# Optimization experiments

Hardware: AMD Instinct MI355X
Metric: run time of the kernel (lower is better)

The kernel has to match this reference:

```python
import jax, jax.numpy as jnp
import numpy as np

B, T, C = 4, 4096, 512
H = 64           # head_size
GRAN = 128       # staircase granularity


def staircase_mask(t, g):
    # tril OR block-diagonal blocks of size g (the staircase fills the upper
    # triangle inside each gxg diagonal block)
    i = jnp.arange(t)
    return (i[:, None] >= i[None, :]) | ((i[:, None] // g) == (i[None, :] // g))


def setup_inputs() -> dict:
    key = jax.random.key(0)
    kx, kk, kq, kv = jax.random.split(key, 4)
    scale = 0.02
    return {
        "x": jax.random.normal(kx, (B, T, C), dtype=jnp.float32),
        "Wk": jax.random.normal(kk, (C, H), dtype=jnp.float32) * scale,
        "Wq": jax.random.normal(kq, (C, H), dtype=jnp.float32) * scale,
        "Wv": jax.random.normal(kv, (C, H), dtype=jnp.float32) * scale,
    }


def reference(x, Wk, Wq, Wv):
    # single head of self-attention with staircase mask (dropout off / eval mode)
    k = x @ Wk          # [B,T,H]
    q = x @ Wq          # [B,T,H]
    v = x @ Wv          # [B,T,H]
    wei = jnp.einsum("bth,bsh->bts", q, k) * (H ** -0.5)   # [B,T,T]
    mask = staircase_mask(T, GRAN)                           # [T,T] bool
    wei = jnp.where(mask, wei, -jnp.inf)
    wei = jax.nn.softmax(wei, axis=-1)
    out = jnp.einsum("bts,bsh->bth", wei, v)                 # [B,T,H]
    return out
```

## Files before the change

kernel.cpp:

```cpp
#include <hip/hip_runtime.h>

typedef unsigned short u16;
typedef unsigned int u32;
typedef unsigned long long u64;
typedef __attribute__((ext_vector_type(8))) short short8;
typedef __attribute__((ext_vector_type(4))) float f32x4;

#define T_ 4096
#define QSCALE 0.18033688f
#define CH 4
#define SBAT 576
#define PSTRIDE 36

#if __has_builtin(__builtin_amdgcn_exp2f)
#define EXP2F(x) __builtin_amdgcn_exp2f(x)
#else
#define EXP2F(x) exp2f(x)
#endif

__device__ __forceinline__ u16 f2bf(float f) {
    unsigned u = __float_as_uint(f);
    u += 0x7FFFu + ((u >> 16) & 1u);
    return (u16)(u >> 16);
}

__global__ __launch_bounds__(256) void wtrans_kernel(
    const float* __restrict__ Wq, const float* __restrict__ Wk,
    const float* __restrict__ Wv, u16* __restrict__ WTf)
{
    const int tid  = blockIdx.x * 256 + threadIdx.x;
    const int frag = tid >> 6;
    const int lane = tid & 63;
    const int ng   = frag >> 4;
    const int kc   = frag & 15;
    const int m    = ng >> 2;
    const float* W = (m == 0) ? Wq : (m == 1) ? Wk : Wv;
    const int h  = (ng & 3) * 16 + (lane & 15);
    const int c0 = kc * 32 + (lane >> 4) * 8;
    short8 v;
    #pragma unroll
    for (int j = 0; j < 8; ++j)
        v[j] = (short)f2bf(W[(c0 + j) * 64 + h]);
    *(short8*)(WTf + (size_t)frag * 512 + lane * 8) = v;
}

__global__ __launch_bounds__(256) void proj_kernel(
    const float* __restrict__ x, const u16* __restrict__ WTf,
    u16* __restrict__ Qf, u16* __restrict__ Kf, u16* __restrict__ Vf)
{
    __shared__ u16 xs[16 * 520];
    __shared__ u16 img[3072];
    const int t    = threadIdx.x;
    const int lane = t & 63;
    const int w    = t >> 6;
    const int l16  = lane & 15;
    const int quad = lane >> 4;
    const int rowbase = blockIdx.x * 16;
    const int bat  = rowbase >> 12;
    const int tloc = rowbase & 4095;

    #pragma unroll
    for (int it = 0; it < 8; ++it) {
        int f   = t + it * 256;
        int row = f >> 7;
        int c4  = (f & 127) * 4;
        f32x4 a = *(const f32x4*)(x + (size_t)(rowbase + row) * 512 + c4);
        unsigned lo = (unsigned)f2bf(a[0]) | ((unsigned)f2bf(a[1]) << 16);
        unsigned hi = (unsigned)f2bf(a[2]) | ((unsigned)f2bf(a[3]) << 16);
        *(uint2*)(xs + row * 520 + c4) = make_uint2(lo, hi);
    }
    __syncthreads();

    f32x4 acc[3];
    #pragma unroll
    for (int nt = 0; nt < 3; ++nt) acc[nt] = (f32x4){0.f, 0.f, 0.f, 0.f};

    const u16* ab = xs + l16 * 520 + quad * 8;
    const u16* wb = WTf + (size_t)(w * 3 * 16) * 512 + lane * 8;

    #pragma unroll 4
    for (int kc = 0; kc < 16; ++kc) {
        short8 af = *(const short8*)(ab + kc * 32);
        #pragma unroll
        for (int nt = 0; nt < 3; ++nt) {
            short8 bf = *(const short8*)(wb + (size_t)(nt * 16 + kc) * 512);
            acc[nt] = __builtin_amdgcn_mfma_f32_16x16x32_bf16(af, bf, acc[nt], 0, 0, 0);
        }
    }

    #pragma unroll
    for (int nt = 0; nt < 3; ++nt) {
        int ng = w * 3 + nt;
        if (ng < 8) {
            int ng4  = ng & 3;
            float sc = (ng < 4) ? QSCALE : 1.0f;
            u16* ib  = img + ((ng < 4) ? 0 : 1024) + (ng4 >> 1) * 512
                          + ((ng4 & 1) * 2 + (l16 >> 3)) * 128 + (l16 & 7);
            #pragma unroll
            for (int i = 0; i < 4; ++i)
                ib[(quad * 4 + i) * 8] = f2bf(acc[nt][i] * sc);
        } else {
            int nt2  = ng - 8;
            unsigned lo = (unsigned)f2bf(acc[nt][0]) | ((unsigned)f2bf(acc[nt][1]) << 16);
            unsigned hi = (unsigned)f2bf(acc[nt][2]) | ((unsigned)f2bf(acc[nt][3]) << 16);
            *(uint2*)(img + 2048 + nt2 * 256 + (quad >> 1) * 128 + l16 * 8
                          + (quad & 1) * 4) = make_uint2(lo, hi);
        }
    }
    __syncthreads();

    const int tb   = tloc >> 4;
    const int kt   = tloc >> 7;
    const int ks   = (tloc >> 5) & 3;
    const int half = (tloc >> 4) & 1;
    uint2 vq = *(uint2*)(img + t * 4);
    uint2 vk = *(uint2*)(img + 1024 + t * 4);
    uint2 vv = *(uint2*)(img + 2048 + t * 4);
    *(uint2*)(Qf + (size_t)(bat * 256 + tb) * 1024 + t * 4) = vq;
    *(uint2*)(Kf + (size_t)(bat * 256 + tb) * 1024 + t * 4) = vk;
    const int nt2c = t >> 6;
    *(uint2*)(Vf + (size_t)((bat * 32 + kt) * 4 + ks) * 2048
                 + nt2c * 512 + half * 256 + (t & 63) * 4) = vv;
}

__global__ __launch_bounds__(256, 4) void attn_kernel(
    const u16* __restrict__ Qf, const u16* __restrict__ Kf,
    const u16* __restrict__ Vf, u32* __restrict__ pnum,
    float* __restrict__ pden, float* __restrict__ out)
{
    __shared__ u16 Ps[4][2][2][16 * PSTRIDE];

    const int w    = threadIdx.x >> 6;
    const int lane = threadIdx.x & 63;
    const int l16  = lane & 15;
    const int qd   = lane >> 4;
    const int xcd  = blockIdx.x & 7;
    const int bat  = xcd >> 1;
    const int tw   = ((blockIdx.x >> 3) * 2 + (xcd & 1)) * 4 + w;

    int A = 31, pre = 0, cc = 1;
    for (;;) {
        cc = (A + CH) / CH;
        int cnt4 = 4 * cc;
        if (tw < pre + cnt4) break;
        pre += cnt4; --A;
    }
    const int r    = tw - pre;
    const int c    = r >> 2;
    const int b_   = r & 3;
    const int nkt  = A + 1;
    const int q32  = 4 * A + b_;
    const int kt0  = c * CH;
    const int kt1  = min(kt0 + CH, nkt);
    const int slot = bat * SBAT + pre + b_ + 4 * c;

    short8 aq[2][2];
    #pragma unroll
    for (int g = 0; g < 2; ++g)
        #pragma unroll
        for (int f = 0; f < 2; ++f)
            aq[g][f] = *(const short8*)(Qf
                + ((size_t)((bat * 256 + q32 * 2 + g) * 2 + f)) * 512 + lane * 8);

    short8 ones;
    #pragma unroll
    for (int j = 0; j < 8; ++j) ones[j] = (short)0x3F80;

    f32x4 acc[2][4];
    f32x4 accden[2];
    #pragma unroll
    for (int g = 0; g < 2; ++g) {
        accden[g] = (f32x4){0.f, 0.f, 0.f, 0.f};
        for (int n = 0; n < 4; ++n) acc[g][n] = (f32x4){0.f, 0.f, 0.f, 0.f};
    }

    u16* Psw = &Ps[w][0][0][0];
    int par = 0;

    short8 ap_prev[2];
    short8 av_prev[4];

    auto step = [&](int kt, int ks, bool first) __attribute__((always_inline)) {
        const u16* kfb = Kf + ((size_t)(bat * 256 + kt * 8) * 2) * 512 + lane * 8;
        const u16* vfb = Vf + ((size_t)((bat * 32 + kt) * 16)) * 512 + lane * 8;
        f32x4 st0g0, st0g1, st1g0, st1g1;
        {
            short8 k0 = *(const short8*)(kfb + (size_t)(2 * ks) * 1024);
            short8 k1 = *(const short8*)(kfb + (size_t)(2 * ks) * 1024 + 512);
            f32x4 s;
            s = (f32x4){0.f, 0.f, 0.f, 0.f};
            s = __builtin_amdgcn_mfma_f32_16x16x32_bf16(k0, aq[0][0], s, 0, 0, 0);
            s = __builtin_amdgcn_mfma_f32_16x16x32_bf16(k1, aq[0][1], s, 0, 0, 0);
            st0g0 = s;
            s = (f32x4){0.f, 0.f, 0.f, 0.f};
            s = __builtin_amdgcn_mfma_f32_16x16x32_bf16(k0, aq[1][0], s, 0, 0, 0);
            s = __builtin_amdgcn_mfma_f32_16x16x32_bf16(k1, aq[1][1], s, 0, 0, 0);
            st0g1 = s;
        }
        {
            short8 k0 = *(const short8*)(kfb + (size_t)(2 * ks + 1) * 1024);
            short8 k1 = *(const short8*)(kfb + (size_t)(2 * ks + 1) * 1024 + 512);
            f32x4 s;
            s = (f32x4){0.f, 0.f, 0.f, 0.f};
            s = __builtin_amdgcn_mfma_f32_16x16x32_bf16(k0, aq[0][0], s, 0, 0, 0);
            s = __builtin_amdgcn_mfma_f32_16x16x32_bf16(k1, aq[0][1], s, 0, 0, 0);
            st1g0 = s;
            s = (f32x4){0.f, 0.f, 0.f, 0.f};
            s = __builtin_amdgcn_mfma_f32_16x16x32_bf16(k0, aq[1][0], s, 0, 0, 0);
            s = __builtin_amdgcn_mfma_f32_16x16x32_bf16(k1, aq[1][1], s, 0, 0, 0);
            st1g1 = s;
        }
        if (!first) {
            accden[0] = __builtin_amdgcn_mfma_f32_16x16x32_bf16(ones, ap_prev[0], accden[0], 0, 0, 0);
            accden[1] = __builtin_amdgcn_mfma_f32_16x16x32_bf16(ones, ap_prev[1], accden[1], 0, 0, 0);
            #pragma unroll
            for (int nt2 = 0; nt2 < 4; ++nt2) {
                acc[0][nt2] = __builtin_amdgcn_mfma_f32_16x16x32_bf16(av_prev[nt2], ap_prev[0], acc[0][nt2], 0, 0, 0);
                acc[1][nt2] = __builtin_amdgcn_mfma_f32_16x16x32_bf16(av_prev[nt2], ap_prev[1], acc[1][nt2], 0, 0, 0);
            }
        }
        u16* sw = Psw + par * 1152;
        #pragma unroll
        for (int b = 0; b < 2; ++b) {
            #pragma unroll
            for (int g = 0; g < 2; ++g) {
                f32x4 s = (b == 0) ? (g == 0 ? st0g0 : st0g1)
                                   : (g == 0 ? st1g0 : st1g1);
                float p0 = EXP2F(s[0]);
                float p1 = EXP2F(s[1]);
                float p2 = EXP2F(s[2]);
                float p3 = EXP2F(s[3]);
                u32 q01 = __builtin_amdgcn_perm(__float_as_uint(p1), __float_as_uint(p0), 0x07060302u);
                u32 q23 = __builtin_amdgcn_perm(__float_as_uint(p3), __float_as_uint(p2), 0x07060302u);
                u64 pv = (u64)q01 | ((u64)q23 << 32);
                *(u64*)(sw + g * 576 + l16 * PSTRIDE + b * 16 + qd * 4) = pv;
            }
        }
        #pragma unroll
        for (int nt2 = 0; nt2 < 4; ++nt2)
            av_prev[nt2] = *(const short8*)(vfb + (size_t)(ks * 4 + nt2) * 512);
        ap_prev[0] = *(const short8*)(sw + 0 * 576 + l16 * PSTRIDE + qd * 8);
        ap_prev[1] = *(const short8*)(sw + 1 * 576 + l16 * PSTRIDE + qd * 8);
        par ^= 1;
    };

    auto body = [&](int kt, bool firstb) __attribute__((always_inline)) {
        step(kt, 0, firstb);
        step(kt, 1, false);
        step(kt, 2, false);
        step(kt, 3, false);
    };

    body(kt0, true);
    if (kt0 + 1 < kt1) body(kt0 + 1, false);
    if (kt0 + 2 < kt1) body(kt0 + 2, false);
    if (kt0 + 3 < kt1) body(kt0 + 3, false);

    accden[0] = __builtin_amdgcn_mfma_f32_16x16x32_bf16(ones, ap_prev[0], accden[0], 0, 0, 0);
    accden[1] = __builtin_amdgcn_mfma_f32_16x16x32_bf16(ones, ap_prev[1], accden[1], 0, 0, 0);
    #pragma unroll
    for (int nt2 = 0; nt2 < 4; ++nt2) {
        acc[0][nt2] = __builtin_amdgcn_mfma_f32_16x16x32_bf16(av_prev[nt2], ap_prev[0], acc[0][nt2], 0, 0, 0);
        acc[1][nt2] = __builtin_amdgcn_mfma_f32_16x16x32_bf16(av_prev[nt2], ap_prev[1], acc[1][nt2], 0, 0, 0);
    }

    float den[2] = { accden[0][0], accden[1][0] };

    if (cc == 1) {
        const float rd0 = 1.0f / den[0];
        const float rd1 = 1.0f / den[1];
        float* op = out + ((size_t)(bat * T_ + q32 * 32 + l16)) * 64 + qd * 4;
        #pragma unroll
        for (int g = 0; g < 2; ++g) {
            const float rd = g ? rd1 : rd0;
            #pragma unroll
            for (int nt2 = 0; nt2 < 4; ++nt2) {
                f32x4 v;
                #pragma unroll
                for (int i = 0; i < 4; ++i) v[i] = acc[g][nt2][i] * rd;
                *(f32x4*)(op + (size_t)g * 16 * 64 + nt2 * 16) = v;
            }
        }
    } else {
        u32* np = pnum + (size_t)slot * 1024;
        #pragma unroll
        for (int g = 0; g < 2; ++g)
            #pragma unroll
            for (int nt2 = 0; nt2 < 4; ++nt2) {
                u32 lo = (u32)f2bf(acc[g][nt2][0]) | ((u32)f2bf(acc[g][nt2][1]) << 16);
                u32 hi = (u32)f2bf(acc[g][nt2][2]) | ((u32)f2bf(acc[g][nt2][3]) << 16);
                u64 val = (u64)lo | ((u64)hi << 32);
                __builtin_nontemporal_store(val, (u64*)(np + (g * 4 + nt2) * 128 + lane * 2));
            }
        if (lane < 32)
            __builtin_nontemporal_store(den[lane >> 4],
                                        &pden[(size_t)slot * 32 + lane]);
    }
}

__global__ __launch_bounds__(256) void fin_kernel(
    const u32* __restrict__ pnum, const float* __restrict__ pden,
    float* __restrict__ out)
{
    __shared__ float sden[8][32];
    __shared__ float rden[32];
    const int blk  = blockIdx.x;
    const int xcd  = blk & 7;
    const int bat  = xcd >> 1;
    const int rest = blk >> 3;
    const int q32  = (rest & 63) * 2 + (xcd & 1);
    const int hh   = rest >> 6;
    const int A = q32 >> 2, b = q32 & 3;
    const int cc = (A + CH) / CH;
    if (cc == 1) return;
    int pre = 0;
    for (int j = 31; j > A; --j) pre += 4 * ((j + CH) / CH);
    const int base = bat * SBAT + pre + b;

    {
        const int md  = threadIdx.x & 31;
        const int grp = threadIdx.x >> 5;
        float d = 0.f;
        for (int ci = grp; ci < cc; ci += 8)
            d += pden[(size_t)(base + 4 * ci) * 32 + md];
        sden[grp][md] = d;
    }
    __syncthreads();
    if (threadIdx.x < 32) {
        float d = 0.f;
        #pragma unroll
        for (int g2 = 0; g2 < 8; ++g2) d += sden[g2][threadIdx.x];
        rden[threadIdx.x] = 1.0f / d;
    }
    __syncthreads();

    const int m   = threadIdx.x >> 3;
    const int g   = m >> 4;
    const int l16 = m & 15;
    const int h0  = hh * 32 + (threadIdx.x & 7) * 4;
    const int nt2 = h0 >> 4;
    const int q0  = (h0 >> 2) & 3;
    const int off = (g * 4 + nt2) * 128 + q0 * 32 + l16 * 2;

    float sv0 = 0.f, sv1 = 0.f, sv2 = 0.f, sv3 = 0.f;
    const u32* sp = pnum + (size_t)base * 1024 + off;
    uint2 cur = *(const uint2*)sp;
    for (int ci = 1; ci < cc; ++ci) {
        uint2 nxt = *(const uint2*)(sp + (size_t)ci * 4096);
        sv0 += __uint_as_float(cur.x << 16);
        sv1 += __uint_as_float(cur.x & 0xFFFF0000u);
        sv2 += __uint_as_float(cur.y << 16);
        sv3 += __uint_as_float(cur.y & 0xFFFF0000u);
        cur = nxt;
    }
    sv0 += __uint_as_float(cur.x << 16);
    sv1 += __uint_as_float(cur.x & 0xFFFF0000u);
    sv2 += __uint_as_float(cur.y << 16);
    sv3 += __uint_as_float(cur.y & 0xFFFF0000u);

    const float rd = rden[m];
    float* op = out + (size_t)(bat * T_ + q32 * 32 + m) * 64 + h0;
    f32x4 r;
    r[0] = sv0 * rd; r[1] = sv1 * rd; r[2] = sv2 * rd; r[3] = sv3 * rd;
    *(f32x4*)op = r;
}

extern "C" void kernel_launch(void* const* d_in, const int* in_sizes, int n_in,
                              void* d_out, int out_size, void* d_ws, size_t ws_size,
                              hipStream_t stream)
{
    const float* x  = (const float*)d_in[0];
    const float* Wk = (const float*)d_in[1];
    const float* Wq = (const float*)d_in[2];
    const float* Wv = (const float*)d_in[3];
    float* out = (float*)d_out;

    u16* ws  = (u16*)d_ws;
    u16* WTf = ws;
    u16* Qf  = ws + 131072;
    u16* Kf  = Qf + 1048576;
    u16* Vf  = Kf + 1048576;
    u32*   pnum = (u32*)(Vf + 1048576);
    float* pden = (float*)(pnum + (size_t)4 * 1088 * 1024);

    wtrans_kernel<<<48, 256, 0, stream>>>(Wq, Wk, Wv, WTf);
    proj_kernel<<<1024, 256, 0, stream>>>(x, WTf, Qf, Kf, Vf);
    attn_kernel<<<SBAT, 256, 0, stream>>>(Qf, Kf, Vf, pnum, pden, out);
    fin_kernel<<<1024, 256, 0, stream>>>(pnum, pden, out);
}
```

Baseline: 116.8 us.

## Process 64 query rows per wave to reuse K/V loads across two q-blocks

Each wave now handles two adjacent 32-row query blocks instead of one, so every K and V fragment loaded from global memory feeds twice as many MFMAs. The grid is halved, the P staging buffer in shared memory doubles, and the launch-bounds occupancy hint drops from 4 to 2 to make room for the larger accumulator register set. The trade-off is fewer waves in flight to hide latency and coarser load balance across the staircase work distribution.

```diff
diff --git a/kernel.cpp b/kernel.cpp
--- a/kernel.cpp
+++ b/kernel.cpp
@@ -10,6 +10,7 @@
 #define QSCALE 0.18033688f
 #define CH 4
 #define SBAT 576
+#define SGRID 288
 #define PSTRIDE 36
 
 #if __has_builtin(__builtin_amdgcn_exp2f)
@@ -123,12 +124,12 @@
                  + nt2c * 512 + half * 256 + (t & 63) * 4) = vv;
 }
 
-__global__ __launch_bounds__(256, 4) void attn_kernel(
+__global__ __launch_bounds__(256, 2) void attn_kernel(
     const u16* __restrict__ Qf, const u16* __restrict__ Kf,
     const u16* __restrict__ Vf, u32* __restrict__ pnum,
     float* __restrict__ pden, float* __restrict__ out)
 {
-    __shared__ u16 Ps[4][2][2][16 * PSTRIDE];
+    __shared__ u16 Ps[4][2][4][16 * PSTRIDE];
 
     const int w    = threadIdx.x >> 6;
     const int lane = threadIdx.x & 63;
@@ -141,91 +142,78 @@
     int A = 31, pre = 0, cc = 1;
     for (;;) {
         cc = (A + CH) / CH;
-        int cnt4 = 4 * cc;
-        if (tw < pre + cnt4) break;
-        pre += cnt4; --A;
+        int cnt2 = 2 * cc;
+        if (tw < pre + cnt2) break;
+        pre += cnt2; --A;
     }
     const int r    = tw - pre;
-    const int c    = r >> 2;
-    const int b_   = r & 3;
+    const int c    = r >> 1;
+    const int bp   = r & 1;
     const int nkt  = A + 1;
-    const int q32  = 4 * A + b_;
+    const int q32a = 4 * A + 2 * bp;
     const int kt0  = c * CH;
     const int kt1  = min(kt0 + CH, nkt);
-    const int slot = bat * SBAT + pre + b_ + 4 * c;
-
-    short8 aq[2][2];
-    #pragma unroll
-    for (int g = 0; g < 2; ++g)
+    const int slot0 = bat * SBAT + 2 * pre + 2 * bp + 4 * c;
+
+    short8 aq[4][2];
+    #pragma unroll
+    for (int gg = 0; gg < 4; ++gg)
         #pragma unroll
         for (int f = 0; f < 2; ++f)
-            aq[g][f] = *(const short8*)(Qf
-                + ((size_t)((bat * 256 + q32 * 2 + g) * 2 + f)) * 512 + lane * 8);
+            aq[gg][f] = *(const short8*)(Qf
+                + ((size_t)((bat * 256 + (q32a + (gg >> 1)) * 2 + (gg & 1)) * 2 + f)) * 512 + lane * 8);
 
     short8 ones;
     #pragma unroll
     for (int j = 0; j < 8; ++j) ones[j] = (short)0x3F80;
 
-    f32x4 acc[2][4];
-    f32x4 accden[2];
-    #pragma unroll
-    for (int g = 0; g < 2; ++g) {
-        accden[g] = (f32x4){0.f, 0.f, 0.f, 0.f};
-        for (int n = 0; n < 4; ++n) acc[g][n] = (f32x4){0.f, 0.f, 0.f, 0.f};
+    f32x4 acc[4][4];
+    f32x4 accden[4];
+    #pragma unroll
+    for (int gg = 0; gg < 4; ++gg) {
+        accden[gg] = (f32x4){0.f, 0.f, 0.f, 0.f};
+        #pragma unroll
+        for (int n = 0; n < 4; ++n) acc[gg][n] = (f32x4){0.f, 0.f, 0.f, 0.f};
     }
 
     u16* Psw = &Ps[w][0][0][0];
     int par = 0;
 
-    short8 ap_prev[2];
+    short8 ap_prev[4];
     short8 av_prev[4];
 
     auto step = [&](int kt, int ks, bool first) __attribute__((always_inline)) {
         const u16* kfb = Kf + ((size_t)(bat * 256 + kt * 8) * 2) * 512 + lane * 8;
         const u16* vfb = Vf + ((size_t)((bat * 32 + kt) * 16)) * 512 + lane * 8;
-        f32x4 st0g0, st0g1, st1g0, st1g1;
-        {
-            short8 k0 = *(const short8*)(kfb + (size_t)(2 * ks) * 1024);
-            short8 k1 = *(const short8*)(kfb + (size_t)(2 * ks) * 1024 + 512);
-            f32x4 s;
-            s = (f32x4){0.f, 0.f, 0.f, 0.f};
-            s = __builtin_amdgcn_mfma_f32_16x16x32_bf16(k0, aq[0][0], s, 0, 0, 0);
-            s = __builtin_amdgcn_mfma_f32_16x16x32_bf16(k1, aq[0][1], s, 0, 0, 0);
-            st0g0 = s;
-            s = (f32x4){0.f, 0.f, 0.f, 0.f};
-            s = __builtin_amdgcn_mfma_f32_16x16x32_bf16(k0, aq[1][0], s, 0, 0, 0);
-            s = __builtin_amdgcn_mfma_f32_16x16x32_bf16(k1, aq[1][1], s, 0, 0, 0);
-            st0g1 = s;
-        }
-        {
-            short8 k0 = *(const short8*)(kfb + (size_t)(2 * ks + 1) * 1024);
-            short8 k1 = *(const short8*)(kfb + (size_t)(2 * ks + 1) * 1024 + 512);
-            f32x4 s;
-            s = (f32x4){0.f, 0.f, 0.f, 0.f};
-            s = __builtin_amdgcn_mfma_f32_16x16x32_bf16(k0, aq[0][0], s, 0, 0, 0);
-            s = __builtin_amdgcn_mfma_f32_16x16x32_bf16(k1, aq[0][1], s, 0, 0, 0);
-            st1g0 = s;
-            s = (f32x4){0.f, 0.f, 0.f, 0.f};
-            s = __builtin_amdgcn_mfma_f32_16x16x32_bf16(k0, aq[1][0], s, 0, 0, 0);
-            s = __builtin_amdgcn_mfma_f32_16x16x32_bf16(k1, aq[1][1], s, 0, 0, 0);
-            st1g1 = s;
+        f32x4 st[2][4];
+        #pragma unroll
+        for (int b = 0; b < 2; ++b) {
+            short8 k0 = *(const short8*)(kfb + (size_t)(2 * ks + b) * 1024);
+            short8 k1 = *(const short8*)(kfb + (size_t)(2 * ks + b) * 1024 + 512);
+            #pragma unroll
+            for (int gg = 0; gg < 4; ++gg) {
+                f32x4 s = (f32x4){0.f, 0.f, 0.f, 0.f};
+                s = __builtin_amdgcn_mfma_f32_16x16x32_bf16(k0, aq[gg][0], s, 0, 0, 0);
+                s = __builtin_amdgcn_mfma_f32_16x16x32_bf16(k1, aq[gg][1], s, 0, 0, 0);
+                st[b][gg] = s;
+            }
         }
         if (!first) {
-            accden[0] = __builtin_amdgcn_mfma_f32_16x16x32_bf16(ones, ap_prev[0], accden[0], 0, 0, 0);
-            accden[1] = __builtin_amdgcn_mfma_f32_16x16x32_bf16(ones, ap_prev[1], accden[1], 0, 0, 0);
-            #pragma unroll
-            for (int nt2 = 0; nt2 < 4; ++nt2) {
-                acc[0][nt2] = __builtin_amdgcn_mfma_f32_16x16x32_bf16(av_prev[nt2], ap_prev[0], acc[0][nt2], 0, 0, 0);
-                acc[1][nt2] = __builtin_amdgcn_mfma_f32_16x16x32_bf16(av_prev[nt2], ap_prev[1], acc[1][nt2], 0, 0, 0);
-            }
-        }
-        u16* sw = Psw + par * 1152;
+            #pragma unroll
+            for (int gg = 0; gg < 4; ++gg)
+                accden[gg] = __builtin_amdgcn_mfma_f32_16x16x32_bf16(ones, ap_prev[gg], accden[gg], 0, 0, 0);
+            #pragma unroll
+            for (int nt2 = 0; nt2 < 4; ++nt2)
+                #pragma unroll
+                for (int gg = 0; gg < 4; ++gg)
+                    acc[gg][nt2] = __builtin_amdgcn_mfma_f32_16x16x32_bf16(av_prev[nt2], ap_prev[gg], acc[gg][nt2], 0, 0, 0);
+        }
+        u16* sw = Psw + par * 2304;
         #pragma unroll
         for (int b = 0; b < 2; ++b) {
             #pragma unroll
-            for (int g = 0; g < 2; ++g) {
-                f32x4 s = (b == 0) ? (g == 0 ? st0g0 : st0g1)
-                                   : (g == 0 ? st1g0 : st1g1);
+            for (int gg = 0; gg < 4; ++gg) {
+                f32x4 s = st[b][gg];
                 float p0 = EXP2F(s[0]);
                 float p1 = EXP2F(s[1]);
                 float p2 = EXP2F(s[2]);
@@ -233,14 +221,15 @@
                 u32 q01 = __builtin_amdgcn_perm(__float_as_uint(p1), __float_as_uint(p0), 0x07060302u);
                 u32 q23 = __builtin_amdgcn_perm(__float_as_uint(p3), __float_as_uint(p2), 0x07060302u);
                 u64 pv = (u64)q01 | ((u64)q23 << 32);
-                *(u64*)(sw + g * 576 + l16 * PSTRIDE + b * 16 + qd * 4) = pv;
+                *(u64*)(sw + gg * 576 + l16 * PSTRIDE + b * 16 + qd * 4) = pv;
             }
         }
         #pragma unroll
         for (int nt2 = 0; nt2 < 4; ++nt2)
             av_prev[nt2] = *(const short8*)(vfb + (size_t)(ks * 4 + nt2) * 512);
-        ap_prev[0] = *(const short8*)(sw + 0 * 576 + l16 * PSTRIDE + qd * 8);
-        ap_prev[1] = *(const short8*)(sw + 1 * 576 + l16 * PSTRIDE + qd * 8);
+        #pragma unroll
+        for (int gg = 0; gg < 4; ++gg)
+            ap_prev[gg] = *(const short8*)(sw + gg * 576 + l16 * PSTRIDE + qd * 8);
         par ^= 1;
     };
 
@@ -256,45 +245,53 @@
     if (kt0 + 2 < kt1) body(kt0 + 2, false);
     if (kt0 + 3 < kt1) body(kt0 + 3, false);
 
-    accden[0] = __builtin_amdgcn_mfma_f32_16x16x32_bf16(ones, ap_prev[0], accden[0], 0, 0, 0);
-    accden[1] = __builtin_amdgcn_mfma_f32_16x16x32_bf16(ones, ap_prev[1], accden[1], 0, 0, 0);
-    #pragma unroll
-    for (int nt2 = 0; nt2 < 4; ++nt2) {
-        acc[0][nt2] = __builtin_amdgcn_mfma_f32_16x16x32_bf16(av_prev[nt2], ap_prev[0], acc[0][nt2], 0, 0, 0);
-        acc[1][nt2] = __builtin_amdgcn_mfma_f32_16x16x32_bf16(av_prev[nt2], ap_prev[1], acc[1][nt2], 0, 0, 0);
-    }
-
-    float den[2] = { accden[0][0], accden[1][0] };
+    #pragma unroll
+    for (int gg = 0; gg < 4; ++gg)
+        accden[gg] = __builtin_amdgcn_mfma_f32_16x16x32_bf16(ones, ap_prev[gg], accden[gg], 0, 0, 0);
+    #pragma unroll
+    for (int nt2 = 0; nt2 < 4; ++nt2)
+        #pragma unroll
+        for (int gg = 0; gg < 4; ++gg)
+            acc[gg][nt2] = __builtin_amdgcn_mfma_f32_16x16x32_bf16(av_prev[nt2], ap_prev[gg], acc[gg][nt2], 0, 0, 0);
+
+    float den[4] = { accden[0][0], accden[1][0], accden[2][0], accden[3][0] };
 
     if (cc == 1) {
-        const float rd0 = 1.0f / den[0];
-        const float rd1 = 1.0f / den[1];
-        float* op = out + ((size_t)(bat * T_ + q32 * 32 + l16)) * 64 + qd * 4;
-        #pragma unroll
-        for (int g = 0; g < 2; ++g) {
-            const float rd = g ? rd1 : rd0;
-            #pragma unroll
-            for (int nt2 = 0; nt2 < 4; ++nt2) {
-                f32x4 v;
+        #pragma unroll
+        for (int j = 0; j < 2; ++j) {
+            float* op = out + ((size_t)(bat * T_ + (q32a + j) * 32 + l16)) * 64 + qd * 4;
+            #pragma unroll
+            for (int g = 0; g < 2; ++g) {
+                const float rd = 1.0f / den[j * 2 + g];
                 #pragma unroll
-                for (int i = 0; i < 4; ++i) v[i] = acc[g][nt2][i] * rd;
-                *(f32x4*)(op + (size_t)g * 16 * 64 + nt2 * 16) = v;
+                for (int nt2 = 0; nt2 < 4; ++nt2) {
+                    f32x4 v;
+                    #pragma unroll
+                    for (int i = 0; i < 4; ++i) v[i] = acc[j * 2 + g][nt2][i] * rd;
+                    *(f32x4*)(op + (size_t)g * 16 * 64 + nt2 * 16) = v;
+                }
             }
         }
     } else {
-        u32* np = pnum + (size_t)slot * 1024;
-        #pragma unroll
-        for (int g = 0; g < 2; ++g)
-            #pragma unroll
-            for (int nt2 = 0; nt2 < 4; ++nt2) {
-                u32 lo = (u32)f2bf(acc[g][nt2][0]) | ((u32)f2bf(acc[g][nt2][1]) << 16);
-                u32 hi = (u32)f2bf(acc[g][nt2][2]) | ((u32)f2bf(acc[g][nt2][3]) << 16);
-                u64 val = (u64)lo | ((u64)hi << 32);
-                __builtin_nontemporal_store(val, (u64*)(np + (g * 4 + nt2) * 128 + lane * 2));
-            }
-        if (lane < 32)
+        #pragma unroll
+        for (int j = 0; j < 2; ++j) {
+            u32* np = pnum + (size_t)(slot0 + j) * 1024;
+            #pragma unroll
+            for (int g = 0; g < 2; ++g)
+                #pragma unroll
+                for (int nt2 = 0; nt2 < 4; ++nt2) {
+                    u32 lo = (u32)f2bf(acc[j * 2 + g][nt2][0]) | ((u32)f2bf(acc[j * 2 + g][nt2][1]) << 16);
+                    u32 hi = (u32)f2bf(acc[j * 2 + g][nt2][2]) | ((u32)f2bf(acc[j * 2 + g][nt2][3]) << 16);
+                    u64 val = (u64)lo | ((u64)hi << 32);
+                    __builtin_nontemporal_store(val, (u64*)(np + (g * 4 + nt2) * 128 + lane * 2));
+                }
+        }
+        if (lane < 32) {
             __builtin_nontemporal_store(den[lane >> 4],
-                                        &pden[(size_t)slot * 32 + lane]);
+                                        &pden[(size_t)slot0 * 32 + lane]);
+            __builtin_nontemporal_store(den[2 + (lane >> 4)],
+                                        &pden[(size_t)(slot0 + 1) * 32 + lane]);
+        }
     }
 }
 
@@ -385,6 +382,6 @@
 
     wtrans_kernel<<<48, 256, 0, stream>>>(Wq, Wk, Wv, WTf);
     proj_kernel<<<1024, 256, 0, stream>>>(x, WTf, Qf, Kf, Vf);
-    attn_kernel<<<SBAT, 256, 0, stream>>>(Qf, Kf, Vf, pnum, pden, out);
+    attn_kernel<<<SGRID, 256, 0, stream>>>(Qf, Kf, Vf, pnum, pden, out);
     fin_kernel<<<1024, 256, 0, stream>>>(pnum, pden, out);
 }
```

After: 114.3 us (median of 2 runs). 2.1% less time.
